# Kernel tuning notes

Hardware: AMD Instinct MI355X
Metric: run time of the kernel (lower is better)

## Reference

```python
import jax, jax.numpy as jnp
import numpy as np
import math

B, L, E, H = 4, 1024, 1024, 16
D = E // H  # head_dim = 64
SCALE = 8.0
EPS = 1e-6

def setup_inputs() -> dict:
    key = jax.random.key(0)
    ks = jax.random.split(key, 16)
    def xavier(k, shape):
        fan_in, fan_out = shape[1], shape[0]
        a = math.sqrt(6.0 / (fan_in + fan_out))
        return jax.random.uniform(k, shape, jnp.float32, -a, a)
    return {
        "query": jax.random.normal(ks[0], (B, L, E), jnp.float32),
        "key": jax.random.normal(ks[1], (B, L, E), jnp.float32),
        "value": jax.random.normal(ks[2], (B, L, E), jnp.float32),
        "attn_mask": jax.random.uniform(ks[3], (B, L), jnp.float32),
        "key_padding_mask": jax.random.randint(ks[4], (B, L), 0, 2) > 0,
        "Wq": xavier(ks[5], (E, E)), "bq": jnp.zeros((E,), jnp.float32),
        "Wk": xavier(ks[6], (E, E)), "bk": jnp.zeros((E,), jnp.float32),
        "Wv": xavier(ks[7], (E, E)), "bv": jnp.zeros((E,), jnp.float32),
        "Wo": xavier(ks[8], (E, E)), "bo": jnp.zeros((E,), jnp.float32),
    }

def reference(query, key, value, attn_mask, key_padding_mask,
              Wq, bq, Wk, bk, Wv, bv, Wo, bo):
    # projections (torch Linear: x @ W.T + b)
    q = (query @ Wq.T + bq).reshape(B, L, H, D).transpose(0, 2, 1, 3)  # (B,H,L,D)
    k = (key @ Wk.T + bk).reshape(B, L, H, D).transpose(0, 2, 1, 3)
    v = (value @ Wv.T + bv).reshape(B, L, H, D).transpose(0, 2, 1, 3)
    scores = jnp.einsum('bhqd,bhkd->bhqk', q, k) / math.sqrt(D)  # (B,H,L,L)
    # soft log-mask bias (training path: no hard -inf at mask==0)
    log_mask = jnp.log(jnp.clip(attn_mask, EPS))  # (B,L)
    scores = scores + SCALE * log_mask[:, None, None, :]
    # key padding mask -> -inf
    scores = jnp.where(key_padding_mask[:, None, None, :], -jnp.inf, scores)
    attn_weights = jax.nn.softmax(scores, axis=-1)  # dropout p=0 -> identity
    attn_output = jnp.einsum('bhqk,bhkd->bhqd', attn_weights, v)
    attn_output = attn_output.transpose(0, 2, 1, 3).reshape(B, L, E)
    attn_output = attn_output @ Wo.T + bo
    return attn_output, attn_weights.mean(axis=1)
```

## Files before the change

### kernel.cpp

```cpp
#include <hip/hip_runtime.h>
#include <math.h>

#define Bsz 4
#define Lq  1024
#define Emb 1024
#define Hh  16
#define Dd  64

#define LOG2E 1.44269504f
#define C2SC  0.18033688f

typedef short bf16x8 __attribute__((ext_vector_type(8)));
typedef float f32x4 __attribute__((ext_vector_type(4)));

static __device__ __forceinline__ unsigned short f2bf(float f) {
    unsigned u = __float_as_uint(f);
    return (unsigned short)((u + 0x7FFFu + ((u >> 16) & 1u)) >> 16);
}
static __device__ __forceinline__ unsigned pack2(float lo, float hi) {
    return __builtin_amdgcn_perm(__float_as_uint(hi) + 0x8000u,
                                 __float_as_uint(lo) + 0x8000u, 0x07060302u);
}

static __device__ __forceinline__ float cross_max(float x) {
    x = fmaxf(x, __shfl_xor(x, 16, 64));
    x = fmaxf(x, __shfl_xor(x, 32, 64));
    return x;
}
static __device__ __forceinline__ float cross_sum(float x) {
    x += __shfl_xor(x, 16, 64);
    x += __shfl_xor(x, 32, 64);
    return x;
}

#define GLOAD_LDS16(gp, lp) __builtin_amdgcn_global_load_lds(                  \
    (const __attribute__((address_space(1))) void*)(gp),                       \
    (__attribute__((address_space(3))) void*)(lp), 16, 0, 0)

__global__ __launch_bounds__(256) void bias_kernel(const float* __restrict__ mask,
                                                   const int* __restrict__ kpm,
                                                   float* __restrict__ bias, int n)
{
    int i = blockIdx.x * 256 + threadIdx.x;
    if (i < n) {
        float b = 8.0f * logf(fmaxf(mask[i], 1e-6f));
        bias[i] = kpm[i] ? -INFINITY : b;
    }
}

__global__ __launch_bounds__(256) void cvt_qkv(const float* __restrict__ q,
                                               const float* __restrict__ k,
                                               const float* __restrict__ v,
                                               unsigned short* __restrict__ qo,
                                               unsigned short* __restrict__ ko,
                                               unsigned short* __restrict__ vo)
{
    int i = blockIdx.x * 256 + threadIdx.x;
    const float* src; unsigned short* dst; int off;
    if (i < 1048576)      { src = q; dst = qo; off = i; }
    else if (i < 2097152) { src = k; dst = ko; off = i - 1048576; }
    else                  { src = v; dst = vo; off = i - 2097152; }
    float4 x = ((const float4*)src)[off];
    ushort4 o;
    o.x = f2bf(x.x); o.y = f2bf(x.y); o.z = f2bf(x.z); o.w = f2bf(x.w);
    ((ushort4*)dst)[off] = o;
}

__global__ __launch_bounds__(256) void cvt_w4(const float* __restrict__ w0,
                                              const float* __restrict__ w1,
                                              const float* __restrict__ w2,
                                              const float* __restrict__ w3,
                                              unsigned short* __restrict__ o0,
                                              unsigned short* __restrict__ o1,
                                              unsigned short* __restrict__ o2,
                                              unsigned short* __restrict__ o3)
{
    int i = blockIdx.x * 256 + threadIdx.x;
    int reg = i >> 18, off = i & 262143;
    const float* src = (reg == 0) ? w0 : (reg == 1) ? w1 : (reg == 2) ? w2 : w3;
    unsigned short* dst = (reg == 0) ? o0 : (reg == 1) ? o1 : (reg == 2) ? o2 : o3;
    float4 x = ((const float4*)src)[off];
    ushort4 o;
    o.x = f2bf(x.x); o.y = f2bf(x.y); o.z = f2bf(x.z); o.w = f2bf(x.w);
    ((ushort4*)dst)[off] = o;
}

__global__ __launch_bounds__(256) void gemm_qkv(const unsigned short* __restrict__ Aq,
                                                const unsigned short* __restrict__ Ak,
                                                const unsigned short* __restrict__ Av,
                                                const unsigned short* __restrict__ Wq,
                                                const unsigned short* __restrict__ Wk,
                                                const unsigned short* __restrict__ Wv,
                                                const float* __restrict__ biq,
                                                const float* __restrict__ bik,
                                                const float* __restrict__ biv,
                                                unsigned short* __restrict__ Oq,
                                                unsigned short* __restrict__ Ok,
                                                unsigned short* __restrict__ Ov)
{
    const int K = 1024;
    __shared__ unsigned short sA[2][64][64];
    __shared__ unsigned short sB[2][128][64];
    int tid = threadIdx.x;
    int w = tid >> 6, lane = tid & 63;

    int bid = blockIdx.x;
    int which = bid >> 9;
    int lin = bid & 511;
    int xcd = lin & 7, idx = lin >> 3;
    int bm = (xcd * 8 + (idx >> 3)) * 64;
    int bn = (idx & 7) * 128;

    const unsigned short* A = (which == 0) ? Aq : (which == 1) ? Ak : Av;
    const unsigned short* Bw = (which == 0) ? Wq : (which == 1) ? Wk : Wv;
    const float* bias = (which == 0) ? biq : (which == 1) ? bik : biv;
    unsigned short* outp = (which == 0) ? Oq : (which == 1) ? Ok : Ov;

    int wr = (w >> 1) * 32, wc = (w & 1) * 64;
    int fr = lane & 15, fg = lane >> 4;
    int csw = fr & 7;

    int srl = lane >> 3;
    int scb = (lane & 7) ^ srl;

    const unsigned short* Ag = A + (size_t)(bm + w * 16 + srl) * K + scb * 8;
    const unsigned short* Bg = Bw + (size_t)(bn + w * 32 + srl) * K + scb * 8;

#define STAGE(BUF, K0) do {                                                      \
    _Pragma("unroll")                                                            \
    for (int j = 0; j < 2; ++j)                                                  \
        GLOAD_LDS16(Ag + (size_t)j * 8 * K + (K0), &sA[BUF][w * 16 + j * 8][0]); \
    _Pragma("unroll")                                                            \
    for (int j = 0; j < 4; ++j)                                                  \
        GLOAD_LDS16(Bg + (size_t)j * 8 * K + (K0), &sB[BUF][w * 32 + j * 8][0]); \
} while (0)

    f32x4 acc[2][4];
#pragma unroll
    for (int i = 0; i < 2; ++i)
#pragma unroll
        for (int j = 0; j < 4; ++j) acc[i][j] = (f32x4){0.f, 0.f, 0.f, 0.f};

    STAGE(0, 0);
    __syncthreads();

#pragma unroll 1
    for (int k0 = 0; k0 < K; k0 += 64) {
        int cur = (k0 >> 6) & 1;
        if (k0 + 64 < K) STAGE(cur ^ 1, k0 + 64);
        bf16x8 af[2][2], bfv[4][2];
#pragma unroll
        for (int i = 0; i < 2; ++i)
#pragma unroll
            for (int kk = 0; kk < 2; ++kk)
                af[i][kk] = *(const bf16x8*)&sA[cur][wr + i * 16 + fr][((kk * 4 + fg) ^ csw) * 8];
#pragma unroll
        for (int j = 0; j < 4; ++j)
#pragma unroll
            for (int kk = 0; kk < 2; ++kk)
                bfv[j][kk] = *(const bf16x8*)&sB[cur][wc + j * 16 + fr][((kk * 4 + fg) ^ csw) * 8];
#pragma unroll
        for (int i = 0; i < 2; ++i)
#pragma unroll
            for (int j = 0; j < 4; ++j) {
                acc[i][j] = __builtin_amdgcn_mfma_f32_16x16x32_bf16(af[i][0], bfv[j][0], acc[i][j], 0, 0, 0);
                acc[i][j] = __builtin_amdgcn_mfma_f32_16x16x32_bf16(af[i][1], bfv[j][1], acc[i][j], 0, 0, 0);
            }
        __syncthreads();
    }
#undef STAGE

    int rb = (lane >> 4) * 4;
#pragma unroll
    for (int j = 0; j < 4; ++j) {
        int n = bn + wc + j * 16 + fr;
        float bia = bias[n];
#pragma unroll
        for (int i = 0; i < 2; ++i) {
#pragma unroll
            for (int r = 0; r < 4; ++r) {
                int m = bm + wr + i * 16 + rb + r;
                float v = acc[i][j][r] + bia;
                int b = m >> 10, l = m & 1023, h = n >> 6, d = n & 63;
                if (which == 2)
                    outp[(((size_t)(b * Hh + h)) * Dd + d) * Lq + l] = f2bf(v);
                else
                    outp[(((size_t)(b * Hh + h)) * Lq + l) * Dd + d] = f2bf(v);
            }
        }
    }
}

__global__ __launch_bounds__(256) void gemm_o(const unsigned short* __restrict__ A,
                                              const unsigned short* __restrict__ Bw,
                                              const float* __restrict__ bias,
                                              float* __restrict__ outp)
{
    const int K = 1024;
    __shared__ unsigned short sA[2][64][64];
    __shared__ unsigned short sB[2][128][64];
    int tid = threadIdx.x;
    int w = tid >> 6, lane = tid & 63;

    int lin = blockIdx.x;
    int xcd = lin & 7, idx = lin >> 3;
    int bm = (xcd * 8 + (idx >> 3)) * 64;
    int bn = (idx & 7) * 128;

    int wr = (w >> 1) * 32, wc = (w & 1) * 64;
    int fr = lane & 15, fg = lane >> 4;
    int csw = fr & 7;

    int srl = lane >> 3;
    int scb = (lane & 7) ^ srl;

    const unsigned short* Ag = A + (size_t)(bm + w * 16 + srl) * K + scb * 8;
    const unsigned short* Bg = Bw + (size_t)(bn + w * 32 + srl) * K + scb * 8;

#define STAGE(BUF, K0) do {                                                      \
    _Pragma("unroll")                                                            \
    for (int j = 0; j < 2; ++j)                                                  \
        GLOAD_LDS16(Ag + (size_t)j * 8 * K + (K0), &sA[BUF][w * 16 + j * 8][0]); \
    _Pragma("unroll")                                                            \
    for (int j = 0; j < 4; ++j)                                                  \
        GLOAD_LDS16(Bg + (size_t)j * 8 * K + (K0), &sB[BUF][w * 32 + j * 8][0]); \
} while (0)

    f32x4 acc[2][4];
#pragma unroll
    for (int i = 0; i < 2; ++i)
#pragma unroll
        for (int j = 0; j < 4; ++j) acc[i][j] = (f32x4){0.f, 0.f, 0.f, 0.f};

    STAGE(0, 0);
    __syncthreads();

#pragma unroll 1
    for (int k0 = 0; k0 < K; k0 += 64) {
        int cur = (k0 >> 6) & 1;
        if (k0 + 64 < K) STAGE(cur ^ 1, k0 + 64);
        bf16x8 af[2][2], bfv[4][2];
#pragma unroll
        for (int i = 0; i < 2; ++i)
#pragma unroll
            for (int kk = 0; kk < 2; ++kk)
                af[i][kk] = *(const bf16x8*)&sA[cur][wr + i * 16 + fr][((kk * 4 + fg) ^ csw) * 8];
#pragma unroll
        for (int j = 0; j < 4; ++j)
#pragma unroll
            for (int kk = 0; kk < 2; ++kk)
                bfv[j][kk] = *(const bf16x8*)&sB[cur][wc + j * 16 + fr][((kk * 4 + fg) ^ csw) * 8];
#pragma unroll
        for (int i = 0; i < 2; ++i)
#pragma unroll
            for (int j = 0; j < 4; ++j) {
                acc[i][j] = __builtin_amdgcn_mfma_f32_16x16x32_bf16(af[i][0], bfv[j][0], acc[i][j], 0, 0, 0);
                acc[i][j] = __builtin_amdgcn_mfma_f32_16x16x32_bf16(af[i][1], bfv[j][1], acc[i][j], 0, 0, 0);
            }
        __syncthreads();
    }
#undef STAGE

    int rb = (lane >> 4) * 4;
#pragma unroll
    for (int j = 0; j < 4; ++j) {
        int n = bn + wc + j * 16 + fr;
        float bia = bias[n];
#pragma unroll
        for (int i = 0; i < 2; ++i)
#pragma unroll
            for (int r = 0; r < 4; ++r) {
                int m = bm + wr + i * 16 + rb + r;
                outp[(size_t)m * 1024 + n] = acc[i][j][r] + bia;
            }
    }
}

__global__ __launch_bounds__(256) void attn_flash(const unsigned short* __restrict__ Qh,
                                                  const unsigned short* __restrict__ Kh,
                                                  const unsigned short* __restrict__ Vt,
                                                  const float* __restrict__ mbias,
                                                  unsigned short* __restrict__ ctx,
                                                  float* __restrict__ mstats,
                                                  float* __restrict__ lstats)
{
    __shared__ float sBias[1024];
    __shared__ unsigned short Wl[4][2][16][64];
    __shared__ unsigned short Kl[2][64][64];
    __shared__ unsigned short Vl[2][64][64];

    int tid = threadIdx.x;
    int w = tid >> 6, lane = tid & 63;
    int fr = lane & 15, fg = lane >> 4;

    int lin = blockIdx.x;
    int xcd = lin & 7, jj = lin >> 3;
    int pair = xcd * 8 + (jj >> 3);
    int qt = jj & 7;
    int b = pair & 3, h = pair >> 2;

    int q0A = qt * 128 + w * 32;
    int q0B = q0A + 16;
    int swz = (fr & 7) << 2;
    int csw = fr & 7;

    const unsigned short* Qp = Qh + ((size_t)(b * Hh + h)) * Lq * Dd;
    const unsigned short* Kp = Kh + ((size_t)(b * Hh + h)) * Lq * Dd;
    const unsigned short* Vp = Vt + ((size_t)(b * Hh + h)) * Dd * Lq;

    int srl = lane >> 3;
    int scb = (lane & 7) ^ srl;

#define STAGEK(BUF, KC) do {                                                     \
    _Pragma("unroll")                                                            \
    for (int i = 0; i < 2; ++i)                                                  \
        GLOAD_LDS16(Kp + (size_t)((KC) + w * 16 + i * 8 + srl) * Dd + scb * 8,   \
                    &Kl[BUF][w * 16 + i * 8][0]);                                \
} while (0)
#define STAGEV(BUF, KC) do {                                                     \
    _Pragma("unroll")                                                            \
    for (int i = 0; i < 2; ++i)                                                  \
        GLOAD_LDS16(Vp + (size_t)(w * 16 + i * 8 + srl) * Lq + (KC) + scb * 8,   \
                    &Vl[BUF][w * 16 + i * 8][0]);                                \
} while (0)

    for (int i = tid; i < 1024; i += 256) sBias[i] = mbias[b * Lq + i] * LOG2E;

    bf16x8 qA0 = *(const bf16x8*)(Qp + (size_t)(q0A + fr) * Dd + fg * 8);
    bf16x8 qA1 = *(const bf16x8*)(Qp + (size_t)(q0A + fr) * Dd + 32 + fg * 8);
    bf16x8 qB0 = *(const bf16x8*)(Qp + (size_t)(q0B + fr) * Dd + fg * 8);
    bf16x8 qB1 = *(const bf16x8*)(Qp + (size_t)(q0B + fr) * Dd + 32 + fg * 8);

    f32x4 OA[4], OB[4];
#pragma unroll
    for (int dt = 0; dt < 4; ++dt) { OA[dt] = (f32x4){0.f,0.f,0.f,0.f}; OB[dt] = (f32x4){0.f,0.f,0.f,0.f}; }
    float mA = -INFINITY, lsA = 0.f, mB = -INFINITY, lsB = 0.f;

    bf16x8 vb0[4], vb1[4];

#define RDK(K0, K1, BUF) do {                                                    \
    _Pragma("unroll")                                                            \
    for (int kt = 0; kt < 4; ++kt) {                                             \
        K0[kt] = *(const bf16x8*)&Kl[BUF][kt * 16 + fr][(fg ^ csw) * 8];         \
        K1[kt] = *(const bf16x8*)&Kl[BUF][kt * 16 + fr][((4 + fg) ^ csw) * 8];   \
    }                                                                            \
} while (0)
#define RDV(BUF) do {                                                            \
    _Pragma("unroll")                                                            \
    for (int dt = 0; dt < 4; ++dt) {                                             \
        vb0[dt] = *(const bf16x8*)&Vl[BUF][dt * 16 + fr][(fg ^ csw) * 8];        \
        vb1[dt] = *(const bf16x8*)&Vl[BUF][dt * 16 + fr][((4 + fg) ^ csw) * 8];  \
    }                                                                            \
} while (0)

#define QK(S, K0, K1, B0, B1) do {                                               \
    _Pragma("unroll")                                                            \
    for (int kt = 0; kt < 4; ++kt) {                                             \
        S[kt] = __builtin_amdgcn_mfma_f32_16x16x32_bf16(K0[kt], B0, (f32x4){0.f,0.f,0.f,0.f}, 0, 0, 0); \
        S[kt] = __builtin_amdgcn_mfma_f32_16x16x32_bf16(K1[kt], B1, S[kt], 0, 0, 0); \
    }                                                                            \
} while (0)

#define SMPV(S, MT, LS, OT, TI, KC) do {                                         \
    float v_[16];                                                                \
    _Pragma("unroll")                                                            \
    for (int kt = 0; kt < 4; ++kt) {                                             \
        float4 bb = *(const float4*)&sBias[(KC) + kt * 16 + fg * 4];             \
        _Pragma("unroll")                                                        \
        for (int r = 0; r < 4; ++r)                                              \
            v_[kt * 4 + r] = S[kt][r] * C2SC + (&bb.x)[r];                       \
    }                                                                            \
    float t8[8];                                                                 \
    _Pragma("unroll")                                                            \
    for (int i = 0; i < 8; ++i) t8[i] = fmaxf(v_[i], v_[i + 8]);                 \
    float t4[4];                                                                 \
    _Pragma("unroll")                                                            \
    for (int i = 0; i < 4; ++i) t4[i] = fmaxf(t8[i], t8[i + 4]);                 \
    float lmax = fmaxf(fmaxf(t4[0], t4[1]), fmaxf(t4[2], t4[3]));                \
    if (!__all(lmax <= MT + 8.f)) {                                              \
        float pm = cross_max(lmax);                                              \
        float mn = fmaxf(MT, pm);                                                \
        float sc = exp2f(MT - mn);                                               \
        LS *= sc;                                                                \
        _Pragma("unroll")                                                        \
        for (int dt = 0; dt < 4; ++dt)                                           \
            _Pragma("unroll")                                                    \
            for (int r = 0; r < 4; ++r) OT[dt][r] *= sc;                         \
        MT = mn;                                                                 \
    }                                                                            \
    _Pragma("unroll")                                                            \
    for (int i = 0; i < 16; ++i) v_[i] = exp2f(v_[i] - MT);                      \
    _Pragma("unroll")                                                            \
    for (int i = 0; i < 8; ++i) t8[i] = v_[i] + v_[i + 8];                       \
    _Pragma("unroll")                                                            \
    for (int i = 0; i < 4; ++i) t4[i] = t8[i] + t8[i + 4];                       \
    LS += (t4[0] + t4[1]) + (t4[2] + t4[3]);                                     \
    _Pragma("unroll")                                                            \
    for (int kt = 0; kt < 4; ++kt) {                                             \
        unsigned w0 = pack2(v_[kt * 4 + 0], v_[kt * 4 + 1]);                     \
        unsigned w1 = pack2(v_[kt * 4 + 2], v_[kt * 4 + 3]);                     \
        uint2 pr; pr.x = w0; pr.y = w1;                                          \
        *(uint2*)&Wl[w][TI][fr][2 * ((kt * 8 + fg * 2) ^ swz)] = pr;             \
    }                                                                            \
    bf16x8 pa0 = *(const bf16x8*)&Wl[w][TI][fr][2 * ((fg * 4) ^ swz)];           \
    bf16x8 pa1 = *(const bf16x8*)&Wl[w][TI][fr][2 * ((16 + fg * 4) ^ swz)];      \
    _Pragma("unroll")                                                            \
    for (int dt = 0; dt < 4; ++dt) {                                             \
        OT[dt] = __builtin_amdgcn_mfma_f32_16x16x32_bf16(vb0[dt], pa0, OT[dt], 0, 0, 0); \
        OT[dt] = __builtin_amdgcn_mfma_f32_16x16x32_bf16(vb1[dt], pa1, OT[dt], 0, 0, 0); \
    }                                                                            \
} while (0)

    STAGEK(0, 0);
    STAGEV(0, 0);
    __syncthreads();

#pragma unroll 1
    for (int c = 0; c < 16; ++c) {
        int cur = c & 1;
        if (c < 15) {
            STAGEK(cur ^ 1, (c + 1) * 64);
            STAGEV(cur ^ 1, (c + 1) * 64);
        }
        bf16x8 k0[4], k1[4];
        RDK(k0, k1, cur);
        f32x4 SA[4], SB[4];
        QK(SA, k0, k1, qA0, qA1);
        QK(SB, k0, k1, qB0, qB1);
        RDV(cur);
        SMPV(SA, mA, lsA, OA, 0, c * 64);
        SMPV(SB, mB, lsB, OB, 1, c * 64);
        __syncthreads();
    }
#undef STAGEK
#undef STAGEV
#undef RDK
#undef RDV
#undef QK
#undef SMPV

    float lAt = cross_sum(lsA), lBt = cross_sum(lsB);
    float liA = 1.f / lAt, liB = 1.f / lBt;
#pragma unroll
    for (int dt = 0; dt < 4; ++dt) {
#pragma unroll
        for (int r = 0; r < 4; ++r) { OA[dt][r] *= liA; OB[dt][r] *= liB; }
    }
#pragma unroll
    for (int dt = 0; dt < 4; ++dt) {
        uint2 pa; pa.x = pack2(OA[dt][0], OA[dt][1]); pa.y = pack2(OA[dt][2], OA[dt][3]);
        *(uint2*)(ctx + ((size_t)(b * Lq + q0A + fr)) * Emb + h * Dd + dt * 16 + fg * 4) = pa;
        uint2 pb; pb.x = pack2(OB[dt][0], OB[dt][1]); pb.y = pack2(OB[dt][2], OB[dt][3]);
        *(uint2*)(ctx + ((size_t)(b * Lq + q0B + fr)) * Emb + h * Dd + dt * 16 + fg * 4) = pb;
    }

    if (lane < 16) {
        mstats[(size_t)(b * Hh + h) * Lq + q0A + lane] = mA;
        lstats[(size_t)(b * Hh + h) * Lq + q0A + lane] = liA;
        mstats[(size_t)(b * Hh + h) * Lq + q0B + lane] = mB;
        lstats[(size_t)(b * Hh + h) * Lq + q0B + lane] = liB;
    }
}

__global__ __launch_bounds__(256) void attn_out2(const unsigned short* __restrict__ Qh,
                                                 const unsigned short* __restrict__ Kh,
                                                 const float* __restrict__ mbias,
                                                 const float* __restrict__ mstats,
                                                 const float* __restrict__ lstats,
                                                 float* __restrict__ out2)
{
    __shared__ unsigned short sQ[2][32][64];
    __shared__ unsigned short sK[2][128][64];
    __shared__ float sM[16][32];
    __shared__ float sLi[16][32];

    int tid = threadIdx.x;
    int w = tid >> 6, lane = tid & 63;
    int fr = lane & 15, fg = lane >> 4;
    int q0 = blockIdx.x * 32;
    int kc = blockIdx.y * 128;
    int b  = blockIdx.z;

    for (int i = tid; i < 512; i += 256) {
        int h = i >> 5, qq = i & 31;
        sM[h][qq]  = mstats[(size_t)(b * Hh + h) * Lq + q0 + qq];
        sLi[h][qq] = lstats[(size_t)(b * Hh + h) * Lq + q0 + qq];
    }

    int srl = lane >> 3;
    int scb = (lane & 7) ^ srl;
    int csw = fr & 7;

#define STAGEH(BUF, H) do {                                                      \
    const unsigned short* Qp_ = Qh + ((size_t)(b * Hh + (H))) * Lq * Dd;         \
    const unsigned short* Kp_ = Kh + ((size_t)(b * Hh + (H))) * Lq * Dd;         \
    GLOAD_LDS16(Qp_ + (size_t)(q0 + w * 8 + srl) * Dd + scb * 8, &sQ[BUF][w * 8][0]); \
    _Pragma("unroll")                                                            \
    for (int i = 0; i < 4; ++i)                                                  \
        GLOAD_LDS16(Kp_ + (size_t)(kc + w * 32 + i * 8 + srl) * Dd + scb * 8,    \
                    &sK[BUF][w * 32 + i * 8][0]);                                \
} while (0)

#define RDH(AQ, BKk, BUF) do {                                                   \
    _Pragma("unroll")                                                            \
    for (int rt = 0; rt < 2; ++rt)                                               \
        _Pragma("unroll")                                                        \
        for (int ks = 0; ks < 2; ++ks)                                           \
            AQ[rt][ks] = *(const bf16x8*)&sQ[BUF][rt * 16 + fr][((ks * 4 + fg) ^ csw) * 8]; \
    _Pragma("unroll")                                                            \
    for (int ct = 0; ct < 2; ++ct)                                               \
        _Pragma("unroll")                                                        \
        for (int ks = 0; ks < 2; ++ks)                                           \
            BKk[ct][ks] = *(const bf16x8*)&sK[BUF][w * 32 + ct * 16 + fr][((ks * 4 + fg) ^ csw) * 8]; \
} while (0)

#define COMPH(AQ, BKk, H) do {                                                   \
    float4 mrow[2], lirow[2];                                                    \
    _Pragma("unroll")                                                            \
    for (int rt = 0; rt < 2; ++rt) {                                             \
        mrow[rt]  = *(const float4*)&sM[(H)][rt * 16 + fg * 4];                  \
        lirow[rt] = *(const float4*)&sLi[(H)][rt * 16 + fg * 4];                 \
    }                                                                            \
    _Pragma("unroll")                                                            \
    for (int rt = 0; rt < 2; ++rt)                                               \
        _Pragma("unroll")                                                        \
        for (int ct = 0; ct < 2; ++ct) {                                         \
            f32x4 s_ = __builtin_amdgcn_mfma_f32_16x16x32_bf16(AQ[rt][0], BKk[ct][0], (f32x4){0.f,0.f,0.f,0.f}, 0, 0, 0); \
            s_ = __builtin_amdgcn_mfma_f32_16x16x32_bf16(AQ[rt][1], BKk[ct][1], s_, 0, 0, 0); \
            float bia = ct ? bias1 : bias0;                                      \
            _Pragma("unroll")                                                    \
            for (int r = 0; r < 4; ++r)                                          \
                o2[rt][ct][r] += exp2f(s_[r] * C2SC + bia - mrow[rt][r]) * lirow[rt][r]; \
        }                                                                        \
} while (0)

    float bias0 = mbias[b * Lq + kc + w * 32 + fr] * LOG2E;
    float bias1 = mbias[b * Lq + kc + w * 32 + 16 + fr] * LOG2E;

    float o2[2][2][4];
#pragma unroll
    for (int rt = 0; rt < 2; ++rt)
#pragma unroll
        for (int ct = 0; ct < 2; ++ct)
#pragma unroll
            for (int r = 0; r < 4; ++r) o2[rt][ct][r] = 0.f;

    STAGEH(0, 0);
    __syncthreads();

#pragma unroll 1
    for (int h = 0; h < Hh; ++h) {
        int cur = h & 1;
        if (h < Hh - 1) STAGEH(cur ^ 1, h + 1);
        bf16x8 aq[2][2], bk[2][2];
        RDH(aq, bk, cur);
        COMPH(aq, bk, h);
        __syncthreads();
    }
#undef STAGEH
#undef RDH
#undef COMPH

#pragma unroll
    for (int rt = 0; rt < 2; ++rt)
#pragma unroll
        for (int ct = 0; ct < 2; ++ct)
#pragma unroll
            for (int r = 0; r < 4; ++r)
                out2[((size_t)(b * Lq + q0 + rt * 16 + fg * 4 + r)) * Lq + kc + w * 32 + ct * 16 + fr]
                    = o2[rt][ct][r] * 0.0625f;
}

extern "C" void kernel_launch(void* const* d_in, const int* in_sizes, int n_in,
                              void* d_out, int out_size, void* d_ws, size_t ws_size,
                              hipStream_t stream)
{
    const float* query = (const float*)d_in[0];
    const float* key   = (const float*)d_in[1];
    const float* value = (const float*)d_in[2];
    const float* amask = (const float*)d_in[3];
    const int*   kpm   = (const int*)d_in[4];
    const float* Wq = (const float*)d_in[5];
    const float* bq = (const float*)d_in[6];
    const float* Wk = (const float*)d_in[7];
    const float* bk = (const float*)d_in[8];
    const float* Wv = (const float*)d_in[9];
    const float* bv = (const float*)d_in[10];
    const float* Wo = (const float*)d_in[11];
    const float* bo = (const float*)d_in[12];

    float* out1 = (float*)d_out;
    float* out2 = out1 + (size_t)Bsz * Lq * Emb;

    const size_t MB = 1u << 20;
    char* ws = (char*)d_ws;
    unsigned short* qbf = (unsigned short*)(ws + 0 * MB);
    unsigned short* kbf = (unsigned short*)(ws + 8 * MB);
    unsigned short* vbf = (unsigned short*)(ws + 16 * MB);
    unsigned short* wqb = (unsigned short*)(ws + 24 * MB);
    unsigned short* wkb = (unsigned short*)(ws + 26 * MB);
    unsigned short* wvb = (unsigned short*)(ws + 28 * MB);
    unsigned short* wob = (unsigned short*)(ws + 30 * MB);
    unsigned short* QhB = (unsigned short*)(ws + 32 * MB);
    unsigned short* KhB = (unsigned short*)(ws + 40 * MB);
    unsigned short* VtB = (unsigned short*)(ws + 48 * MB);
    unsigned short* ctxB = (unsigned short*)(ws + 56 * MB);
    float* mbias  = (float*)(ws + 64 * MB);
    float* mstats = (float*)(ws + 0 * MB);
    float* lstats = (float*)(ws + 0 * MB + 256 * 1024);

    bias_kernel<<<16, 256, 0, stream>>>(amask, kpm, mbias, Bsz * Lq);

    cvt_qkv<<<12288, 256, 0, stream>>>(query, key, value, qbf, kbf, vbf);
    cvt_w4<<<4096, 256, 0, stream>>>(Wq, Wk, Wv, Wo, wqb, wkb, wvb, wob);

    gemm_qkv<<<1536, 256, 0, stream>>>(qbf, kbf, vbf, wqb, wkb, wvb,
                                       bq, bk, bv, QhB, KhB, VtB);

    attn_flash<<<512, 256, 0, stream>>>(QhB, KhB, VtB, mbias, ctxB, mstats, lstats);
    attn_out2<<<dim3(32, 8, 4), 256, 0, stream>>>(QhB, KhB, mbias, mstats, lstats, out2);

    gemm_o<<<512, 256, 0, stream>>>(ctxB, wob, bo, out1);
}
```

Before: 168.2 us.

## Halve per-block query tile in flash attention and drop lazy rescale

```diff
diff --git a/kernel.cpp b/kernel.cpp
--- a/kernel.cpp
+++ b/kernel.cpp
@@ -285,7 +285,7 @@
                                                   float* __restrict__ lstats)
 {
     __shared__ float sBias[1024];
-    __shared__ unsigned short Wl[4][2][16][64];
+    __shared__ unsigned short Wl[4][16][64];
     __shared__ unsigned short Kl[2][64][64];
     __shared__ unsigned short Vl[2][64][64];
 
@@ -295,12 +295,11 @@
 
     int lin = blockIdx.x;
     int xcd = lin & 7, jj = lin >> 3;
-    int pair = xcd * 8 + (jj >> 3);
-    int qt = jj & 7;
+    int pair = xcd * 8 + (jj >> 4);
+    int qt = jj & 15;
     int b = pair & 3, h = pair >> 2;
 
-    int q0A = qt * 128 + w * 32;
-    int q0B = q0A + 16;
+    int q0 = qt * 64 + w * 16;
     int swz = (fr & 7) << 2;
     int csw = fr & 7;
 
@@ -326,15 +325,13 @@
 
     for (int i = tid; i < 1024; i += 256) sBias[i] = mbias[b * Lq + i] * LOG2E;
 
-    bf16x8 qA0 = *(const bf16x8*)(Qp + (size_t)(q0A + fr) * Dd + fg * 8);
-    bf16x8 qA1 = *(const bf16x8*)(Qp + (size_t)(q0A + fr) * Dd + 32 + fg * 8);
-    bf16x8 qB0 = *(const bf16x8*)(Qp + (size_t)(q0B + fr) * Dd + fg * 8);
-    bf16x8 qB1 = *(const bf16x8*)(Qp + (size_t)(q0B + fr) * Dd + 32 + fg * 8);
-
-    f32x4 OA[4], OB[4];
-#pragma unroll
-    for (int dt = 0; dt < 4; ++dt) { OA[dt] = (f32x4){0.f,0.f,0.f,0.f}; OB[dt] = (f32x4){0.f,0.f,0.f,0.f}; }
-    float mA = -INFINITY, lsA = 0.f, mB = -INFINITY, lsB = 0.f;
+    bf16x8 q0f = *(const bf16x8*)(Qp + (size_t)(q0 + fr) * Dd + fg * 8);
+    bf16x8 q1f = *(const bf16x8*)(Qp + (size_t)(q0 + fr) * Dd + 32 + fg * 8);
+
+    f32x4 O[4];
+#pragma unroll
+    for (int dt = 0; dt < 4; ++dt) O[dt] = (f32x4){0.f, 0.f, 0.f, 0.f};
+    float m_r = -INFINITY, ls = 0.f;
 
     bf16x8 vb0[4], vb1[4];
 
@@ -353,15 +350,15 @@
     }                                                                            \
 } while (0)
 
-#define QK(S, K0, K1, B0, B1) do {                                               \
+#define QK(S, K0, K1) do {                                                       \
     _Pragma("unroll")                                                            \
     for (int kt = 0; kt < 4; ++kt) {                                             \
-        S[kt] = __builtin_amdgcn_mfma_f32_16x16x32_bf16(K0[kt], B0, (f32x4){0.f,0.f,0.f,0.f}, 0, 0, 0); \
-        S[kt] = __builtin_amdgcn_mfma_f32_16x16x32_bf16(K1[kt], B1, S[kt], 0, 0, 0); \
+        S[kt] = __builtin_amdgcn_mfma_f32_16x16x32_bf16(K0[kt], q0f, (f32x4){0.f,0.f,0.f,0.f}, 0, 0, 0); \
+        S[kt] = __builtin_amdgcn_mfma_f32_16x16x32_bf16(K1[kt], q1f, S[kt], 0, 0, 0); \
     }                                                                            \
 } while (0)
 
-#define SMPV(S, MT, LS, OT, TI, KC) do {                                         \
+#define SMPV(S, KC) do {                                                         \
     float v_[16];                                                                \
     _Pragma("unroll")                                                            \
     for (int kt = 0; kt < 4; ++kt) {                                             \
@@ -376,38 +373,37 @@
     float t4[4];                                                                 \
     _Pragma("unroll")                                                            \
     for (int i = 0; i < 4; ++i) t4[i] = fmaxf(t8[i], t8[i + 4]);                 \
-    float lmax = fmaxf(fmaxf(t4[0], t4[1]), fmaxf(t4[2], t4[3]));                \
-    if (!__all(lmax <= MT + 8.f)) {                                              \
-        float pm = cross_max(lmax);                                              \
-        float mn = fmaxf(MT, pm);                                                \
-        float sc = exp2f(MT - mn);                                               \
-        LS *= sc;                                                                \
+    float pmax = fmaxf(fmaxf(t4[0], t4[1]), fmaxf(t4[2], t4[3]));                \
+    pmax = cross_max(pmax);                                                      \
+    float mn = fmaxf(m_r, pmax);                                                 \
+    float sc = exp2f(m_r - mn);                                                  \
+    _Pragma("unroll")                                                            \
+    for (int i = 0; i < 16; ++i) v_[i] = exp2f(v_[i] - mn);                      \
+    float cs;                                                                    \
+    _Pragma("unroll")                                                            \
+    for (int i = 0; i < 8; ++i) t8[i] = v_[i] + v_[i + 8];                       \
+    _Pragma("unroll")                                                            \
+    for (int i = 0; i < 4; ++i) t4[i] = t8[i] + t8[i + 4];                       \
+    cs = (t4[0] + t4[1]) + (t4[2] + t4[3]);                                      \
+    ls = ls * sc + cs;                                                           \
+    m_r = mn;                                                                    \
+    _Pragma("unroll")                                                            \
+    for (int dt = 0; dt < 4; ++dt)                                               \
         _Pragma("unroll")                                                        \
-        for (int dt = 0; dt < 4; ++dt)                                           \
-            _Pragma("unroll")                                                    \
-            for (int r = 0; r < 4; ++r) OT[dt][r] *= sc;                         \
-        MT = mn;                                                                 \
-    }                                                                            \
-    _Pragma("unroll")                                                            \
-    for (int i = 0; i < 16; ++i) v_[i] = exp2f(v_[i] - MT);                      \
-    _Pragma("unroll")                                                            \
-    for (int i = 0; i < 8; ++i) t8[i] = v_[i] + v_[i + 8];                       \
-    _Pragma("unroll")                                                            \
-    for (int i = 0; i < 4; ++i) t4[i] = t8[i] + t8[i + 4];                       \
-    LS += (t4[0] + t4[1]) + (t4[2] + t4[3]);                                     \
+        for (int r = 0; r < 4; ++r) O[dt][r] *= sc;                              \
     _Pragma("unroll")                                                            \
     for (int kt = 0; kt < 4; ++kt) {                                             \
         unsigned w0 = pack2(v_[kt * 4 + 0], v_[kt * 4 + 1]);                     \
         unsigned w1 = pack2(v_[kt * 4 + 2], v_[kt * 4 + 3]);                     \
         uint2 pr; pr.x = w0; pr.y = w1;                                          \
-        *(uint2*)&Wl[w][TI][fr][2 * ((kt * 8 + fg * 2) ^ swz)] = pr;             \
+        *(uint2*)&Wl[w][fr][2 * ((kt * 8 + fg * 2) ^ swz)] = pr;                 \
     }                                                                            \
-    bf16x8 pa0 = *(const bf16x8*)&Wl[w][TI][fr][2 * ((fg * 4) ^ swz)];           \
-    bf16x8 pa1 = *(const bf16x8*)&Wl[w][TI][fr][2 * ((16 + fg * 4) ^ swz)];      \
+    bf16x8 pa0 = *(const bf16x8*)&Wl[w][fr][2 * ((fg * 4) ^ swz)];               \
+    bf16x8 pa1 = *(const bf16x8*)&Wl[w][fr][2 * ((16 + fg * 4) ^ swz)];          \
     _Pragma("unroll")                                                            \
     for (int dt = 0; dt < 4; ++dt) {                                             \
-        OT[dt] = __builtin_amdgcn_mfma_f32_16x16x32_bf16(vb0[dt], pa0, OT[dt], 0, 0, 0); \
-        OT[dt] = __builtin_amdgcn_mfma_f32_16x16x32_bf16(vb1[dt], pa1, OT[dt], 0, 0, 0); \
+        O[dt] = __builtin_amdgcn_mfma_f32_16x16x32_bf16(vb0[dt], pa0, O[dt], 0, 0, 0); \
+        O[dt] = __builtin_amdgcn_mfma_f32_16x16x32_bf16(vb1[dt], pa1, O[dt], 0, 0, 0); \
     }                                                                            \
 } while (0)
 
@@ -424,12 +420,10 @@
         }
         bf16x8 k0[4], k1[4];
         RDK(k0, k1, cur);
-        f32x4 SA[4], SB[4];
-        QK(SA, k0, k1, qA0, qA1);
-        QK(SB, k0, k1, qB0, qB1);
+        f32x4 SA[4];
+        QK(SA, k0, k1);
         RDV(cur);
-        SMPV(SA, mA, lsA, OA, 0, c * 64);
-        SMPV(SB, mB, lsB, OB, 1, c * 64);
+        SMPV(SA, c * 64);
         __syncthreads();
     }
 #undef STAGEK
@@ -439,26 +433,22 @@
 #undef QK
 #undef SMPV
 
-    float lAt = cross_sum(lsA), lBt = cross_sum(lsB);
-    float liA = 1.f / lAt, liB = 1.f / lBt;
+    float lt = cross_sum(ls);
+    float li = 1.f / lt;
+#pragma unroll
+    for (int dt = 0; dt < 4; ++dt)
+#pragma unroll
+        for (int r = 0; r < 4; ++r) O[dt][r] *= li;
+
 #pragma unroll
     for (int dt = 0; dt < 4; ++dt) {
-#pragma unroll
-        for (int r = 0; r < 4; ++r) { OA[dt][r] *= liA; OB[dt][r] *= liB; }
-    }
-#pragma unroll
-    for (int dt = 0; dt < 4; ++dt) {
-        uint2 pa; pa.x = pack2(OA[dt][0], OA[dt][1]); pa.y = pack2(OA[dt][2], OA[dt][3]);
-        *(uint2*)(ctx + ((size_t)(b * Lq + q0A + fr)) * Emb + h * Dd + dt * 16 + fg * 4) = pa;
-        uint2 pb; pb.x = pack2(OB[dt][0], OB[dt][1]); pb.y = pack2(OB[dt][2], OB[dt][3]);
-        *(uint2*)(ctx + ((size_t)(b * Lq + q0B + fr)) * Emb + h * Dd + dt * 16 + fg * 4) = pb;
+        uint2 pa; pa.x = pack2(O[dt][0], O[dt][1]); pa.y = pack2(O[dt][2], O[dt][3]);
+        *(uint2*)(ctx + ((size_t)(b * Lq + q0 + fr)) * Emb + h * Dd + dt * 16 + fg * 4) = pa;
     }
 
     if (lane < 16) {
-        mstats[(size_t)(b * Hh + h) * Lq + q0A + lane] = mA;
-        lstats[(size_t)(b * Hh + h) * Lq + q0A + lane] = liA;
-        mstats[(size_t)(b * Hh + h) * Lq + q0B + lane] = mB;
-        lstats[(size_t)(b * Hh + h) * Lq + q0B + lane] = liB;
+        mstats[(size_t)(b * Hh + h) * Lq + q0 + lane] = m_r;
+        lstats[(size_t)(b * Hh + h) * Lq + q0 + lane] = li;
     }
 }
 
@@ -617,7 +607,7 @@
     gemm_qkv<<<1536, 256, 0, stream>>>(qbf, kbf, vbf, wqb, wkb, wvb,
                                        bq, bk, bv, QhB, KhB, VtB);
 
-    attn_flash<<<512, 256, 0, stream>>>(QhB, KhB, VtB, mbias, ctxB, mstats, lstats);
+    attn_flash<<<1024, 256, 0, stream>>>(QhB, KhB, VtB, mbias, ctxB, mstats, lstats);
     attn_out2<<<dim3(32, 8, 4), 256, 0, stream>>>(QhB, KhB, mbias, mstats, lstats, out2);
 
     gemm_o<<<512, 256, 0, stream>>>(ctxB, wob, bo, out1);
```

Measured after the change: 172.7 us. +2.7%, slower.
